# Kernel tuning notes

Hardware: AMD Instinct MI355X
Metric: run time of the kernel (lower is better)

Reference implementation:

```python
import jax, jax.numpy as jnp
import numpy as np

E = 768      # image_embedding
H = 12       # attention_head
DH = E // H  # head_dim = 64; NOTE: seq_len MUST equal DH for this module's math
S = DH       # seq_len = 64
B = 1024
HID = 3072   # hidden_layer
EPS = 1e-6


def setup_inputs() -> dict:
    key = jax.random.key(0)
    ks = jax.random.split(key, 12)
    sd = 0.02
    return {
        "image": jax.random.normal(ks[0], (B, S, E), dtype=jnp.float32),
        # single shared LayerNorm (used before both attention and MLP)
        "ln_g": jnp.ones((E,), dtype=jnp.float32),
        "ln_b": jnp.zeros((E,), dtype=jnp.float32),
        # Q/K/V linears, stored as [in, out]
        "Wq": jax.random.normal(ks[1], (E, E), dtype=jnp.float32) * sd,
        "bq": jnp.zeros((E,), dtype=jnp.float32),
        "Wk": jax.random.normal(ks[2], (E, E), dtype=jnp.float32) * sd,
        "bk": jnp.zeros((E,), dtype=jnp.float32),
        "Wv": jax.random.normal(ks[3], (E, E), dtype=jnp.float32) * sd,
        "bv": jnp.zeros((E,), dtype=jnp.float32),
        # MLP
        "W1": jax.random.normal(ks[4], (E, HID), dtype=jnp.float32) * sd,
        "b1": jnp.zeros((HID,), dtype=jnp.float32),
        "W2": jax.random.normal(ks[5], (HID, E), dtype=jnp.float32) * sd,
        "b2": jnp.zeros((E,), dtype=jnp.float32),
    }


def _layernorm(x, g, b):
    mu = jnp.mean(x, axis=-1, keepdims=True)
    var = jnp.mean(jnp.square(x - mu), axis=-1, keepdims=True)
    return (x - mu) * jax.lax.rsqrt(var + EPS) * g + b


def _heads(x):  # [B,S,E] -> [B,H,S,DH]
    b, s, _ = x.shape
    return x.reshape(b, s, H, DH).transpose(0, 2, 1, 3)


def reference(image, ln_g, ln_b, Wq, bq, Wk, bk, Wv, bv, W1, b1, W2, b2):
    b, s, e = image.shape
    # --- attention branch (pre-norm, shared LN) ---
    hn = _layernorm(image, ln_g, ln_b)
    q = _heads(hn @ Wq + bq)  # [B,H,S,DH]
    k = _heads(hn @ Wk + bk)
    v = _heads(hn @ Wv + bv)
    # NOTE: original scales by sqrt(embed_dim), NOT sqrt(head_dim)
    score = jax.nn.softmax(jnp.einsum("bhsd,bhtd->bhst", q, k) / jnp.sqrt(jnp.float32(e)), axis=-1)
    # NOTE: original computes value @ score (not score @ value): [B,H,S,DH]@[B,H,S,S]
    # requires DH == S; then reshapes [B,H,S,S] directly to [B,S,E]
    attn = jnp.einsum("bhsd,bhdt->bhst", v, score).reshape(b, s, e)
    x = image + attn
    # --- MLP branch (same shared LN; dropout=0 in eval) ---
    hn2 = _layernorm(x, ln_g, ln_b)
    mlp = jax.nn.gelu(hn2 @ W1 + b1, approximate=False) @ W2 + b2
    return x + mlp
```

## Files before the change

kernel.cpp:

```cpp
#include <hip/hip_runtime.h>
#include <hip/hip_bf16.h>
#include <cstdint>
#include <cstddef>


typedef __bf16 bf16;
typedef __bf16 bf16x8 __attribute__((ext_vector_type(8)));
typedef __bf16 bf16x4 __attribute__((ext_vector_type(4)));
typedef float  f32x4  __attribute__((ext_vector_type(4)));

#define LDS_ASYNC16(lds, g)                                                     \
  __builtin_amdgcn_global_load_lds(                                             \
      (const __attribute__((address_space(1))) void*)(g),                       \
      (__attribute__((address_space(3))) void*)(lds), 16, 0, 0)

#define NROWS 65536
#define E_DIM 768
#define HID_DIM 3072
#define HEADS 12
#define QKV_N 2304

__global__ __launch_bounds__(256) void transpose_cast(
    const float* __restrict__ in, bf16* __restrict__ out, int K, int N) {
  __shared__ float tile[32][33];
  int tx = threadIdx.x & 31, ty = threadIdx.x >> 5;
  int n0 = blockIdx.x * 32, k0 = blockIdx.y * 32;
#pragma unroll
  for (int i = 0; i < 4; ++i)
    tile[ty + 8 * i][tx] = in[(size_t)(k0 + ty + 8 * i) * N + n0 + tx];
  __syncthreads();
#pragma unroll
  for (int i = 0; i < 4; ++i)
    out[(size_t)(n0 + ty + 8 * i) * K + k0 + tx] = (bf16)tile[tx][ty + 8 * i];
}

__global__ __launch_bounds__(256) void pack_bias(
    const float* __restrict__ bq, const float* __restrict__ bk,
    const float* __restrict__ bv, float* __restrict__ o) {
  int i = blockIdx.x * 256 + threadIdx.x;
  const float* src = i < 768 ? bq : (i < 1536 ? bk : bv);
  o[i] = src[i & 767];
}

__global__ __launch_bounds__(256) void ln_kernel(
    const float* __restrict__ x, const float* __restrict__ gam,
    const float* __restrict__ bet, bf16* __restrict__ out) {
  int row  = blockIdx.x * 4 + (threadIdx.x >> 6);
  int lane = threadIdx.x & 63;
  const float4* xr = (const float4*)(x + (size_t)row * E_DIM);
  float4 v[3];
  float s = 0.f, ss = 0.f;
#pragma unroll
  for (int i = 0; i < 3; ++i) {
    v[i] = xr[lane + 64 * i];
    s  += v[i].x + v[i].y + v[i].z + v[i].w;
    ss += v[i].x * v[i].x + v[i].y * v[i].y + v[i].z * v[i].z + v[i].w * v[i].w;
  }
#pragma unroll
  for (int m = 1; m < 64; m <<= 1) {
    s  += __shfl_xor(s, m);
    ss += __shfl_xor(ss, m);
  }
  float mean = s * (1.f / 768.f);
  float var  = ss * (1.f / 768.f) - mean * mean;
  float rstd = rsqrtf(var + 1e-6f);
  bf16x4* o = (bf16x4*)(out + (size_t)row * E_DIM);
#pragma unroll
  for (int i = 0; i < 3; ++i) {
    float4 g4 = ((const float4*)gam)[lane + 64 * i];
    float4 b4 = ((const float4*)bet)[lane + 64 * i];
    bf16x4 r;
    r[0] = (bf16)((v[i].x - mean) * rstd * g4.x + b4.x);
    r[1] = (bf16)((v[i].y - mean) * rstd * g4.y + b4.y);
    r[2] = (bf16)((v[i].z - mean) * rstd * g4.z + b4.z);
    r[3] = (bf16)((v[i].w - mean) * rstd * g4.w + b4.w);
    o[lane + 64 * i] = r;
  }
}

__global__ __launch_bounds__(256) void attn_kernel(
    const bf16* __restrict__ qkv, const float* __restrict__ image,
    float* __restrict__ xout) {
  __shared__ __align__(16) bf16 qs[64 * 72];
  __shared__ __align__(16) bf16 ks[64 * 72];
  __shared__ __align__(16) bf16 vs[64 * 72];
  __shared__ __align__(16) bf16 pT[64 * 72];

  const int t = threadIdx.x, w = t >> 6, lane = t & 63;
  const int quad = lane >> 4, l15 = lane & 15;
  const int h = blockIdx.x % HEADS, b = blockIdx.x / HEADS;

  const bf16* base = qkv + (size_t)(b * 64) * QKV_N + h * 64;
#pragma unroll
  for (int i = 0; i < 2; ++i) {
    int slot = i * 256 + t;
    int row = slot >> 3, c = (slot & 7) * 8;
    size_t go = (size_t)row * QKV_N + c;
    *(bf16x8*)&qs[row * 72 + c] = *(const bf16x8*)&base[go];
    *(bf16x8*)&ks[row * 72 + c] = *(const bf16x8*)&base[go + 768];
    *(bf16x8*)&vs[row * 72 + c] = *(const bf16x8*)&base[go + 1536];
  }
  __syncthreads();

  f32x4 sc[4] = {};
#pragma unroll
  for (int kk = 0; kk < 2; ++kk) {
    bf16x8 af = *(const bf16x8*)&qs[(w * 16 + l15) * 72 + kk * 32 + quad * 8];
#pragma unroll
    for (int ni = 0; ni < 4; ++ni) {
      bf16x8 bfr = *(const bf16x8*)&ks[(ni * 16 + l15) * 72 + kk * 32 + quad * 8];
      sc[ni] = __builtin_amdgcn_mfma_f32_16x16x32_bf16(af, bfr, sc[ni], 0, 0, 0);
    }
  }

  const float inv_sqrt_e = 0.03608439182435161f;
#pragma unroll
  for (int r = 0; r < 4; ++r) {
    float s0 = sc[0][r] * inv_sqrt_e, s1 = sc[1][r] * inv_sqrt_e;
    float s2 = sc[2][r] * inv_sqrt_e, s3 = sc[3][r] * inv_sqrt_e;
    float mx = fmaxf(fmaxf(s0, s1), fmaxf(s2, s3));
    mx = fmaxf(mx, __shfl_xor(mx, 1));
    mx = fmaxf(mx, __shfl_xor(mx, 2));
    mx = fmaxf(mx, __shfl_xor(mx, 4));
    mx = fmaxf(mx, __shfl_xor(mx, 8));
    float e0 = __expf(s0 - mx), e1 = __expf(s1 - mx);
    float e2 = __expf(s2 - mx), e3 = __expf(s3 - mx);
    float sm = e0 + e1 + e2 + e3;
    sm += __shfl_xor(sm, 1);
    sm += __shfl_xor(sm, 2);
    sm += __shfl_xor(sm, 4);
    sm += __shfl_xor(sm, 8);
    float inv = 1.f / sm;
    sc[0][r] = e0 * inv; sc[1][r] = e1 * inv;
    sc[2][r] = e2 * inv; sc[3][r] = e3 * inv;
  }

#pragma unroll
  for (int ni = 0; ni < 4; ++ni) {
    int tc = ni * 16 + l15;
#pragma unroll
    for (int r = 0; r < 4; ++r) {
      int s = w * 16 + quad * 4 + r;
      pT[tc * 72 + s] = (bf16)sc[ni][r];
    }
  }
  __syncthreads();

  f32x4 ao[4] = {};
#pragma unroll
  for (int kk = 0; kk < 2; ++kk) {
    bf16x8 af = *(const bf16x8*)&vs[(w * 16 + l15) * 72 + kk * 32 + quad * 8];
#pragma unroll
    for (int ni = 0; ni < 4; ++ni) {
      bf16x8 bfr = *(const bf16x8*)&pT[(ni * 16 + l15) * 72 + kk * 32 + quad * 8];
      ao[ni] = __builtin_amdgcn_mfma_f32_16x16x32_bf16(af, bfr, ao[ni], 0, 0, 0);
    }
  }

  size_t base_o = (size_t)b * 49152 + (size_t)h * 4096;
#pragma unroll
  for (int ni = 0; ni < 4; ++ni) {
    int tc = ni * 16 + l15;
#pragma unroll
    for (int r = 0; r < 4; ++r) {
      int s = w * 16 + quad * 4 + r;
      size_t off = base_o + (size_t)s * 64 + tc;
      xout[off] = image[off] + ao[ni][r];
    }
  }
}

__device__ inline float gelu_f(float x) {
  float u = x * (0.7978845608028654f + 0.0356774081f * x * x);
  float e = __expf(2.f * u);
  float th = 1.f - 2.f / (e + 1.f);
  return 0.5f * x * (1.f + th);
}

template <int EPI>
__global__ __launch_bounds__(256) void gemm_bt(
    const bf16* __restrict__ A, const bf16* __restrict__ B,
    const float* __restrict__ bias, bf16* __restrict__ outb, float* outf,
    const float* resid, int M, int N, int K) {
  __shared__ __align__(16) bf16 As[128 * 32];
  __shared__ __align__(16) bf16 Bs[128 * 32];
  const int t = threadIdx.x, w = t >> 6, lane = t & 63;
  const int quad = lane >> 4, l15 = lane & 15;
  const int wm = w >> 1, wn = w & 1;

  const int Nt = gridDim.x;
  int flat = blockIdx.x + Nt * blockIdx.y;
  int xcd = flat & 7, rest = flat >> 3;
  int bn = rest % Nt, bm = (rest / Nt) * 8 + xcd;

  const bf16* Ag = A + (size_t)bm * 128 * K;
  const bf16* Bg = B + (size_t)bn * 128 * K;

  f32x4 acc[4][4] = {};
  const int swz = (l15 >> 1) & 3;

  for (int k0 = 0; k0 < K; k0 += 32) {
    __syncthreads();
#pragma unroll
    for (int c = 0; c < 2; ++c) {
      int slot = c * 256 + t;
      int row = slot >> 2;
      int cg = (slot & 3) ^ ((row >> 1) & 3);
      size_t go = (size_t)row * K + k0 + cg * 8;
      int lo = (c * 256 + w * 64) * 16;
      LDS_ASYNC16((char*)As + lo, Ag + go);
      LDS_ASYNC16((char*)Bs + lo, Bg + go);
    }
    __syncthreads();
    bf16x8 af[4], bfr[4];
#pragma unroll
    for (int i = 0; i < 4; ++i) {
      af[i]  = *(const bf16x8*)&As[(wm * 64 + i * 16 + l15) * 32 + (quad ^ swz) * 8];
      bfr[i] = *(const bf16x8*)&Bs[(wn * 64 + i * 16 + l15) * 32 + (quad ^ swz) * 8];
    }
#pragma unroll
    for (int mi = 0; mi < 4; ++mi)
#pragma unroll
      for (int ni = 0; ni < 4; ++ni)
        acc[mi][ni] = __builtin_amdgcn_mfma_f32_16x16x32_bf16(
            af[mi], bfr[ni], acc[mi][ni], 0, 0, 0);
  }

  const int row0 = bm * 128 + wm * 64, col0 = bn * 128 + wn * 64;
#pragma unroll
  for (int mi = 0; mi < 4; ++mi) {
#pragma unroll
    for (int ni = 0; ni < 4; ++ni) {
      int col = col0 + ni * 16 + l15;
      float bc = bias[col];
#pragma unroll
      for (int r = 0; r < 4; ++r) {
        int row = row0 + mi * 16 + quad * 4 + r;
        float v = acc[mi][ni][r] + bc;
        size_t off = (size_t)row * N + col;
        if (EPI == 0) {
          outb[off] = (bf16)gelu_f(v);
        } else if (EPI == 1) {
          outf[off] = resid[off] + v;
        } else {
          outb[off] = (bf16)v;
        }
      }
    }
  }
}

extern "C" void kernel_launch(void* const* d_in, const int* in_sizes, int n_in,
                              void* d_out, int out_size, void* d_ws,
                              size_t ws_size, hipStream_t stream) {
  const float* image = (const float*)d_in[0];
  const float* ln_g  = (const float*)d_in[1];
  const float* ln_b  = (const float*)d_in[2];
  const float* Wq    = (const float*)d_in[3];
  const float* bq    = (const float*)d_in[4];
  const float* Wk    = (const float*)d_in[5];
  const float* bk    = (const float*)d_in[6];
  const float* Wv    = (const float*)d_in[7];
  const float* bv    = (const float*)d_in[8];
  const float* W1    = (const float*)d_in[9];
  const float* b1    = (const float*)d_in[10];
  const float* W2    = (const float*)d_in[11];
  const float* b2    = (const float*)d_in[12];
  float* out = (float*)d_out;

  char* ws = (char*)d_ws;
  bf16* hn   = (bf16*)ws;  ws += (size_t)NROWS * E_DIM * 2;
  bf16* h1   = (bf16*)ws;
  bf16* qkv  = (bf16*)ws;  ws += (size_t)NROWS * HID_DIM * 2;
  bf16* WqkvT = (bf16*)ws; ws += (size_t)QKV_N * E_DIM * 2;
  bf16* W1T  = (bf16*)ws;  ws += (size_t)E_DIM * HID_DIM * 2;
  bf16* W2T  = (bf16*)ws;  ws += (size_t)E_DIM * HID_DIM * 2;
  float* bqkv = (float*)ws; ws += QKV_N * 4;

  dim3 blk(256);
  transpose_cast<<<dim3(24, 24), blk, 0, stream>>>(Wq, WqkvT, 768, 768);
  transpose_cast<<<dim3(24, 24), blk, 0, stream>>>(Wk, WqkvT + 768 * 768, 768, 768);
  transpose_cast<<<dim3(24, 24), blk, 0, stream>>>(Wv, WqkvT + 2 * 768 * 768, 768, 768);
  transpose_cast<<<dim3(96, 24), blk, 0, stream>>>(W1, W1T, 768, 3072);
  transpose_cast<<<dim3(24, 96), blk, 0, stream>>>(W2, W2T, 3072, 768);
  pack_bias<<<dim3(9), blk, 0, stream>>>(bq, bk, bv, bqkv);

  ln_kernel<<<NROWS / 4, blk, 0, stream>>>(image, ln_g, ln_b, hn);
  gemm_bt<2><<<dim3(QKV_N / 128, NROWS / 128), blk, 0, stream>>>(
      hn, WqkvT, bqkv, qkv, nullptr, nullptr, NROWS, QKV_N, E_DIM);
  attn_kernel<<<1024 * HEADS, blk, 0, stream>>>(qkv, image, out);
  ln_kernel<<<NROWS / 4, blk, 0, stream>>>(out, ln_g, ln_b, hn);
  gemm_bt<0><<<dim3(HID_DIM / 128, NROWS / 128), blk, 0, stream>>>(
      hn, W1T, b1, h1, nullptr, nullptr, NROWS, HID_DIM, E_DIM);
  gemm_bt<1><<<dim3(E_DIM / 128, NROWS / 128), blk, 0, stream>>>(
      h1, W2T, b2, nullptr, out, out, NROWS, E_DIM, HID_DIM);
}
```

Baseline: 1.956 ms.

## Replace 128x128 GEMM with 256x256 tile, double-buffered, phase-interleaved async pipeline

Replaces the simple 128x128x32 GEMM, which synchronises twice per k-step, with a 512-thread 256x256x64 kernel. It double-buffers 128KB of LDS and issues async global-to-LDS loads of the next stage, interleaved across four MFMA phases with explicit vmcnt/lgkmcnt waits and priority hints. It also changes the XCD-aware block remapping and the XOR LDS swizzle. This is meant to raise arithmetic intensity and hide load latency behind MFMA work, at the cost of one workgroup per CU (the LDS use) and tricky wait-count correctness.

```diff
diff --git a/kernel.cpp b/kernel.cpp
--- a/kernel.cpp
+++ b/kernel.cpp
@@ -177,74 +177,137 @@
   return 0.5f * x * (1.f + th);
 }
 
+__device__ __forceinline__ f32x4 mfma8(bf16x8 a, bf16x8 b, f32x4 c) {
+  return __builtin_amdgcn_mfma_f32_16x16x32_bf16(a, b, c, 0, 0, 0);
+}
+
+#define LDF(P, OFF) (*(const bf16x8*)((P) + (OFF)))
+
 template <int EPI>
-__global__ __launch_bounds__(256) void gemm_bt(
+__global__ __launch_bounds__(512) void gemm256(
     const bf16* __restrict__ A, const bf16* __restrict__ B,
     const float* __restrict__ bias, bf16* __restrict__ outb, float* outf,
     const float* resid, int M, int N, int K) {
-  __shared__ __align__(16) bf16 As[128 * 32];
-  __shared__ __align__(16) bf16 Bs[128 * 32];
-  const int t = threadIdx.x, w = t >> 6, lane = t & 63;
+  __shared__ __align__(16) char lds[131072];
+  const int t = threadIdx.x;
+  const int wq = t >> 6, lane = t & 63;
   const int quad = lane >> 4, l15 = lane & 15;
-  const int wm = w >> 1, wn = w & 1;
-
-  const int Nt = gridDim.x;
-  int flat = blockIdx.x + Nt * blockIdx.y;
-  int xcd = flat & 7, rest = flat >> 3;
-  int bn = rest % Nt, bm = (rest / Nt) * 8 + xcd;
-
-  const bf16* Ag = A + (size_t)bm * 128 * K;
-  const bf16* Bg = B + (size_t)bn * 128 * K;
-
-  f32x4 acc[4][4] = {};
-  const int swz = (l15 >> 1) & 3;
-
-  for (int k0 = 0; k0 < K; k0 += 32) {
-    __syncthreads();
-#pragma unroll
-    for (int c = 0; c < 2; ++c) {
-      int slot = c * 256 + t;
-      int row = slot >> 2;
-      int cg = (slot & 3) ^ ((row >> 1) & 3);
-      size_t go = (size_t)row * K + k0 + cg * 8;
-      int lo = (c * 256 + w * 64) * 16;
-      LDS_ASYNC16((char*)As + lo, Ag + go);
-      LDS_ASYNC16((char*)Bs + lo, Bg + go);
-    }
-    __syncthreads();
-    bf16x8 af[4], bfr[4];
-#pragma unroll
-    for (int i = 0; i < 4; ++i) {
-      af[i]  = *(const bf16x8*)&As[(wm * 64 + i * 16 + l15) * 32 + (quad ^ swz) * 8];
-      bfr[i] = *(const bf16x8*)&Bs[(wn * 64 + i * 16 + l15) * 32 + (quad ^ swz) * 8];
-    }
-#pragma unroll
-    for (int mi = 0; mi < 4; ++mi)
-#pragma unroll
-      for (int ni = 0; ni < 4; ++ni)
-        acc[mi][ni] = __builtin_amdgcn_mfma_f32_16x16x32_bf16(
-            af[mi], bfr[ni], acc[mi][ni], 0, 0, 0);
-  }
-
-  const int row0 = bm * 128 + wm * 64, col0 = bn * 128 + wn * 64;
-#pragma unroll
-  for (int mi = 0; mi < 4; ++mi) {
+  const int wm = wq >> 2, wn = wq & 3;
+
+  const int Ntile = (int)gridDim.x;
+  const int nwg = Ntile * (int)gridDim.y;
+  const int flat = (int)blockIdx.y * Ntile + (int)blockIdx.x;
+  const int id2 = (flat & 7) * (nwg >> 3) + (flat >> 3);
+  const int bn = id2 % Ntile, bm = id2 / Ntile;
+
+  const int NT = K >> 6;
+  const size_t rowK = (size_t)K;
+
+  const int tr = t >> 3, ts = t & 7;
+  const bf16* aSrc = A + ((size_t)bm * 256 + tr) * rowK + ((ts ^ (tr & 7)) << 3);
+  const bf16* bSrc = B + ((size_t)bn * 256 + tr) * rowK + ((ts ^ (tr & 7)) << 3);
+
+  char* ldsA = (char*)lds;
+  char* ldsB = (char*)lds + 65536;
+  const int stDst = wq * 1024;
+
+#define STAGE_H(LB, BUFP, H, SRC, KT)                                           \
+  do {                                                                          \
+    LDS_ASYNC16((LB) + (BUFP) * 32768 + ((H) * 128 + 0) * 128 + stDst,          \
+                (SRC) + (size_t)((H) * 128 + 0) * rowK + (size_t)(KT) * 64);    \
+    LDS_ASYNC16((LB) + (BUFP) * 32768 + ((H) * 128 + 64) * 128 + stDst,         \
+                (SRC) + (size_t)((H) * 128 + 64) * rowK + (size_t)(KT) * 64);   \
+  } while (0)
+
+  STAGE_H(ldsA, 0, 0, aSrc, 0);
+  STAGE_H(ldsA, 0, 1, aSrc, 0);
+  STAGE_H(ldsB, 0, 0, bSrc, 0);
+  STAGE_H(ldsB, 0, 1, bSrc, 0);
+  STAGE_H(ldsA, 1, 0, aSrc, 1);
+  STAGE_H(ldsA, 1, 1, aSrc, 1);
+  STAGE_H(ldsB, 1, 0, bSrc, 1);
+  STAGE_H(ldsB, 1, 1, bSrc, 1);
+  asm volatile("s_waitcnt vmcnt(8)" ::: "memory");
+  __builtin_amdgcn_s_barrier();
+
+  const int sx = l15 & 7;
+  const int c0 = (quad ^ sx) << 4;
+  const int c1 = ((4 + quad) ^ sx) << 4;
+  const int arow = (wm * 64 + l15) * 128;
+  const int brow = (wn * 64 + l15) * 128;
+
+  f32x4 acc[8][4] = {};
+  bf16x8 bReg[4][2];
+
+#define GPHASE(OFF0, OFF1, M0, STAGE_STMT, TAIL_STMT)                           \
+  do {                                                                          \
+    bf16x8 a00 = LDF(Ab, (OFF0) + c0);                                          \
+    bf16x8 a01 = LDF(Ab, (OFF0) + c1);                                          \
+    bf16x8 a10 = LDF(Ab, (OFF1) + c0);                                          \
+    bf16x8 a11 = LDF(Ab, (OFF1) + c1);                                          \
+    STAGE_STMT;                                                                 \
+    asm volatile("" ::: "memory");                                              \
+    __builtin_amdgcn_s_barrier();                                               \
+    asm volatile("s_waitcnt lgkmcnt(0)" ::: "memory");                          \
+    __builtin_amdgcn_s_setprio(1);                                              \
+    _Pragma("unroll")                                                           \
+    for (int ni = 0; ni < 4; ++ni) {                                            \
+      acc[(M0)][ni]     = mfma8(a00, bReg[ni][0], acc[(M0)][ni]);               \
+      acc[(M0)][ni]     = mfma8(a01, bReg[ni][1], acc[(M0)][ni]);               \
+      acc[(M0) + 1][ni] = mfma8(a10, bReg[ni][0], acc[(M0) + 1][ni]);           \
+      acc[(M0) + 1][ni] = mfma8(a11, bReg[ni][1], acc[(M0) + 1][ni]);           \
+    }                                                                           \
+    __builtin_amdgcn_s_setprio(0);                                              \
+    TAIL_STMT;                                                                  \
+    __builtin_amdgcn_s_barrier();                                               \
+  } while (0)
+
+  for (int g = 0; g < NT; ++g) {
+    const int bufp = g & 1;
+    const char* Ab = ldsA + bufp * 32768;
+    const char* Bb = ldsB + bufp * 32768;
+    const int kn = g + 1, bnx = kn & 1;
+
 #pragma unroll
     for (int ni = 0; ni < 4; ++ni) {
-      int col = col0 + ni * 16 + l15;
-      float bc = bias[col];
+      bReg[ni][0] = LDF(Bb, brow + ni * 2048 + c0);
+      bReg[ni][1] = LDF(Bb, brow + ni * 2048 + c1);
+    }
+    GPHASE(arow, arow + 2048, 0,
+           { if (g >= 1 && kn < NT) STAGE_H(ldsA, bnx, 1, aSrc, kn); }, {});
+    GPHASE(arow + 4096, arow + 6144, 2,
+           { if (g >= 1 && kn < NT) STAGE_H(ldsB, bnx, 0, bSrc, kn); }, {});
+    GPHASE(arow + 16384, arow + 18432, 4,
+           { if (g >= 1 && kn < NT) STAGE_H(ldsB, bnx, 1, bSrc, kn); }, {});
+    GPHASE(arow + 20480, arow + 22528, 6,
+           { if (g + 2 < NT) STAGE_H(ldsA, bufp, 0, aSrc, g + 2); },
+           {
+             if (g < NT - 2)
+               asm volatile("s_waitcnt vmcnt(2)" ::: "memory");
+             else if (g == NT - 2)
+               asm volatile("s_waitcnt vmcnt(0)" ::: "memory");
+           });
+  }
+#undef GPHASE
+#undef STAGE_H
+
+  const int row0 = bm * 256 + wm * 64 + quad * 4;
+  const int col0 = bn * 256 + wn * 64 + l15;
+#pragma unroll
+  for (int mi = 0; mi < 8; ++mi) {
+    const int rbase = row0 + (mi >> 2) * 128 + (mi & 3) * 16;
+#pragma unroll
+    for (int ni = 0; ni < 4; ++ni) {
+      const int col = col0 + ni * 16;
+      const float bc = bias[col];
 #pragma unroll
       for (int r = 0; r < 4; ++r) {
-        int row = row0 + mi * 16 + quad * 4 + r;
-        float v = acc[mi][ni][r] + bc;
-        size_t off = (size_t)row * N + col;
-        if (EPI == 0) {
-          outb[off] = (bf16)gelu_f(v);
-        } else if (EPI == 1) {
-          outf[off] = resid[off] + v;
-        } else {
-          outb[off] = (bf16)v;
-        }
+        const int row = rbase + r;
+        const float v = acc[mi][ni][r] + bc;
+        const size_t off = (size_t)row * N + col;
+        if (EPI == 0)      outb[off] = (bf16)gelu_f(v);
+        else if (EPI == 1) outf[off] = resid[off] + v;
+        else               outb[off] = (bf16)v;
       }
     }
   }
@@ -278,6 +341,7 @@
   float* bqkv = (float*)ws; ws += QKV_N * 4;
 
   dim3 blk(256);
+  dim3 blk512(512);
   transpose_cast<<<dim3(24, 24), blk, 0, stream>>>(Wq, WqkvT, 768, 768);
   transpose_cast<<<dim3(24, 24), blk, 0, stream>>>(Wk, WqkvT + 768 * 768, 768, 768);
   transpose_cast<<<dim3(24, 24), blk, 0, stream>>>(Wv, WqkvT + 2 * 768 * 768, 768, 768);
@@ -286,12 +350,12 @@
   pack_bias<<<dim3(9), blk, 0, stream>>>(bq, bk, bv, bqkv);
 
   ln_kernel<<<NROWS / 4, blk, 0, stream>>>(image, ln_g, ln_b, hn);
-  gemm_bt<2><<<dim3(QKV_N / 128, NROWS / 128), blk, 0, stream>>>(
+  gemm256<2><<<dim3(QKV_N / 256, NROWS / 256), blk512, 0, stream>>>(
       hn, WqkvT, bqkv, qkv, nullptr, nullptr, NROWS, QKV_N, E_DIM);
   attn_kernel<<<1024 * HEADS, blk, 0, stream>>>(qkv, image, out);
   ln_kernel<<<NROWS / 4, blk, 0, stream>>>(out, ln_g, ln_b, hn);
-  gemm_bt<0><<<dim3(HID_DIM / 128, NROWS / 128), blk, 0, stream>>>(
+  gemm256<0><<<dim3(HID_DIM / 256, NROWS / 256), blk512, 0, stream>>>(
       hn, W1T, b1, h1, nullptr, nullptr, NROWS, HID_DIM, E_DIM);
-  gemm_bt<1><<<dim3(E_DIM / 128, NROWS / 128), blk, 0, stream>>>(
+  gemm256<1><<<dim3(E_DIM / 256, NROWS / 256), blk512, 0, stream>>>(
       h1, W2T, b2, nullptr, out, out, NROWS, E_DIM, HID_DIM);
 }
```

Measured after the change: 1.609 ms. 17.8% less time.
